# Performance work log

Measured on AMD Instinct MI355X. Metric: run time of the kernel, lower is better.

The kernel has to match this reference:

```python
import jax, jax.numpy as jnp
import numpy as np

B, T, D = 2, 2048, 1024
H, HD = 16, 64  # num_heads, key_size

def setup_inputs() -> dict:
    key = jax.random.key(0)
    ks = jax.random.split(key, 5)
    s = 1.0 / np.sqrt(D)  # VarianceScaling(1.0, fan_in) approx
    return {
        "query": jax.random.normal(ks[0], (B, T, D), dtype=jnp.float32),
        "wq": jax.random.normal(ks[1], (D, H * HD), dtype=jnp.float32) * s,
        "bq": jnp.zeros((H * HD,), dtype=jnp.float32),
        "wk": jax.random.normal(ks[2], (D, H * HD), dtype=jnp.float32) * s,
        "bk": jnp.zeros((H * HD,), dtype=jnp.float32),
        "wv": jax.random.normal(ks[3], (D, H * HD), dtype=jnp.float32) * s,
        "bv": jnp.zeros((H * HD,), dtype=jnp.float32),
        "wo": jax.random.normal(ks[4], (H * HD, D), dtype=jnp.float32) * (1.0 / np.sqrt(H * HD)),
        "bo": jnp.zeros((D,), dtype=jnp.float32),
    }

def reference(query, wq, bq, wk, bk, wv, bv, wo, bo):
    b, t, _ = query.shape
    proj = lambda w, bias: (query @ w + bias).reshape(b, t, H, HD)
    q = proj(wq, bq) / np.sqrt(HD).astype(np.float32)  # fixed scaling on queries
    k = proj(wk, bk)
    v = proj(wv, bv)
    logits = jnp.einsum('bthd,bThd->bhtT', q, k)  # [B,H,T,T]
    causal = jnp.tril(jnp.ones((t, t), dtype=logits.dtype))
    logits = logits - 1e10 * (1.0 - causal)
    weights = jax.nn.softmax(logits, axis=-1)
    attn = jnp.einsum('bhtT,bThd->bthd', weights, v)
    attn_vec = attn.reshape(b, t, H * HD)
    return attn_vec @ wo + bo
```

## Files before the change

kernel.cpp:

```cpp
#include <hip/hip_runtime.h>
#include <hip/hip_bf16.h>
#include <stdint.h>
#include <math.h>

typedef short bf16x8 __attribute__((ext_vector_type(8)));
typedef float f32x4 __attribute__((ext_vector_type(4)));
typedef __hip_bfloat16 bf16;

#define MFMA16(a, b, c) __builtin_amdgcn_mfma_f32_16x16x32_bf16((a), (b), (c), 0, 0, 0)

__device__ __forceinline__ void glds16(const void* g, void* l) {
  __builtin_amdgcn_global_load_lds((const __attribute__((address_space(1))) void*)g,
                                   (__attribute__((address_space(3))) void*)l, 16, 0, 0);
}

__device__ __forceinline__ bf16x8 ld8(const bf16* p) {
  return *reinterpret_cast<const bf16x8*>(p);
}


__global__ void k_cvt_x(const float* __restrict__ x, bf16* __restrict__ o, int n4) {
  int i = blockIdx.x * blockDim.x + threadIdx.x;
  if (i < n4) {
    float4 v = reinterpret_cast<const float4*>(x)[i];
    bf16 a0 = __float2bfloat16(v.x), a1 = __float2bfloat16(v.y);
    bf16 a2 = __float2bfloat16(v.z), a3 = __float2bfloat16(v.w);
    ushort4 r;
    r.x = reinterpret_cast<unsigned short&>(a0);
    r.y = reinterpret_cast<unsigned short&>(a1);
    r.z = reinterpret_cast<unsigned short&>(a2);
    r.w = reinterpret_cast<unsigned short&>(a3);
    reinterpret_cast<ushort4*>(o)[i] = r;
  }
}

__global__ void k_transpose_cvt(const float* __restrict__ wq, const float* __restrict__ wk,
                                const float* __restrict__ wv, const float* __restrict__ wo,
                                bf16* __restrict__ Wqkvt, bf16* __restrict__ Wot) {
  __shared__ float tile[32][33];
  const int z = blockIdx.z;
  const float* src = (z == 0) ? wq : (z == 1) ? wk : (z == 2) ? wv : wo;
  bf16* dst = (z < 3) ? (Wqkvt + (size_t)z * 1024 * 1024) : Wot;
  const int tx = threadIdx.x & 31, ty = threadIdx.x >> 5;
  const int x = blockIdx.x * 32 + tx;
  const int y0 = blockIdx.y * 32;
#pragma unroll
  for (int i = 0; i < 4; ++i) tile[ty + i * 8][tx] = src[(size_t)(y0 + ty + i * 8) * 1024 + x];
  __syncthreads();
#pragma unroll
  for (int i = 0; i < 4; ++i) {
    int c = blockIdx.x * 32 + ty + i * 8;
    dst[(size_t)c * 1024 + y0 + tx] = __float2bfloat16(tile[tx][ty + i * 8]);
  }
}


__device__ __forceinline__ void gemm_core(const bf16* __restrict__ A, const bf16* __restrict__ Bt,
                                          int K, int arow0, int bcol0,
                                          bf16* As, bf16* Bs, f32x4 acc[4][4]) {
  const int tid = threadIdx.x, lane = tid & 63, w = tid >> 6;
  const int rsub = lane >> 3, slot = lane & 7;
  const int srcslot = slot ^ rsub;
  const int wrow = (w >> 1) * 64, wcol = (w & 1) * 64;
  const int lr = lane & 15, lg = lane >> 4;
  const int nkt = K >> 6;
  for (int kt = 0; kt < nkt; ++kt) {
    const int k0 = kt * 64;
    if (kt) __syncthreads();
#pragma unroll
    for (int i = 0; i < 4; ++i) {
      const int chunk = w * 4 + i;
      glds16(A + (size_t)(arow0 + chunk * 8 + rsub) * K + k0 + srcslot * 8, As + chunk * 512);
      glds16(Bt + (size_t)(bcol0 + chunk * 8 + rsub) * K + k0 + srcslot * 8, Bs + chunk * 512);
    }
    __syncthreads();
#pragma unroll
    for (int kk = 0; kk < 2; ++kk) {
      bf16x8 af[4], bfv[4];
#pragma unroll
      for (int m = 0; m < 4; ++m) {
        const int row = wrow + m * 16 + lr;
        const int byte = (row * 128 + ((kk * 32 + lg * 8) << 1)) ^ ((row & 7) << 4);
        af[m] = *reinterpret_cast<const bf16x8*>(reinterpret_cast<const char*>(As) + byte);
      }
#pragma unroll
      for (int n = 0; n < 4; ++n) {
        const int row = wcol + n * 16 + lr;
        const int byte = (row * 128 + ((kk * 32 + lg * 8) << 1)) ^ ((row & 7) << 4);
        bfv[n] = *reinterpret_cast<const bf16x8*>(reinterpret_cast<const char*>(Bs) + byte);
      }
#pragma unroll
      for (int m = 0; m < 4; ++m)
#pragma unroll
        for (int n = 0; n < 4; ++n) acc[m][n] = MFMA16(af[m], bfv[n], acc[m][n]);
    }
  }
}


__global__ __launch_bounds__(256) void k_gemm_qkv(
    const bf16* __restrict__ X, const bf16* __restrict__ Wt,
    const float* __restrict__ bq, const float* __restrict__ bk, const float* __restrict__ bv,
    bf16* __restrict__ Qo, bf16* __restrict__ Ko, bf16* __restrict__ Vt) {
  __shared__ bf16 As[128 * 64], Bs[128 * 64];
  f32x4 acc[4][4];
#pragma unroll
  for (int i = 0; i < 4; ++i)
#pragma unroll
    for (int j = 0; j < 4; ++j) acc[i][j] = (f32x4){0.f, 0.f, 0.f, 0.f};
  const int arow0 = blockIdx.y * 128, bcol0 = blockIdx.x * 128;
  gemm_core(X, Wt, 1024, arow0, bcol0, As, Bs, acc);
  const int lane = threadIdx.x & 63, w = threadIdx.x >> 6;
  const int wrow = (w >> 1) * 64, wcol = (w & 1) * 64;
  const int lr = lane & 15, lg = lane >> 4;
  const float QSCALE = 0.125f * 1.4426950408889634f;
#pragma unroll
  for (int mi = 0; mi < 4; ++mi) {
#pragma unroll
    for (int ni = 0; ni < 4; ++ni) {
      const int r0 = arow0 + wrow + mi * 16 + lg * 4;
      const int col = bcol0 + wcol + ni * 16 + lr;
      const int which = col >> 10, cw = col & 1023, h = cw >> 6, hd = cw & 63;
      const int b = r0 >> 11, t0 = r0 & 2047;
      if (which == 2) {
        const float bias = bv[cw];
        ushort4 pk;
#pragma unroll
        for (int j = 0; j < 4; ++j) {
          bf16 hv = __float2bfloat16(acc[mi][ni][j] + bias);
          reinterpret_cast<unsigned short*>(&pk)[j] = reinterpret_cast<unsigned short&>(hv);
        }
        *reinterpret_cast<ushort4*>(Vt + ((size_t)((b * 16 + h) * 64 + hd)) * 2048 + t0) = pk;
      } else {
        const float bias = which ? bk[cw] : bq[cw];
        const float scale = which ? 1.0f : QSCALE;
        bf16* dst = which ? Ko : Qo;
#pragma unroll
        for (int j = 0; j < 4; ++j) {
          float v = (acc[mi][ni][j] + bias) * scale;
          dst[((size_t)((b * 16 + h) * 2048) + t0 + j) * 64 + hd] = __float2bfloat16(v);
        }
      }
    }
  }
}


__global__ __launch_bounds__(256) void k_attn(const bf16* __restrict__ Q, const bf16* __restrict__ Kc,
                                              const bf16* __restrict__ Vt, bf16* __restrict__ attn) {
  __shared__ bf16 Ks[2][64 * 64];
  __shared__ bf16 Vs[2][64 * 64];
  __shared__ bf16 Plds[4][16 * 64];
  const int lane = threadIdx.x & 63, w = threadIdx.x >> 6;
  const int lr = lane & 15, lg = lane >> 4;
  const int rsub = lane >> 3, slot = lane & 7;
  const int srcslot = slot ^ rsub;
  const int bh = blockIdx.x;
  const int qt = 31 - blockIdx.y;
  const int b = bh >> 4, h = bh & 15;
  const bf16* Qp = Q + (size_t)bh * 2048 * 64;
  const bf16* Kp = Kc + (size_t)bh * 2048 * 64;
  const bf16* Vp = Vt + (size_t)bh * 64 * 2048;

  const int q0 = qt * 64 + w * 16;
  const bf16x8 qa0 = ld8(Qp + (size_t)(q0 + lr) * 64 + lg * 8);
  const bf16x8 qa1 = ld8(Qp + (size_t)(q0 + lr) * 64 + 32 + lg * 8);
  f32x4 o[4];
#pragma unroll
  for (int n = 0; n < 4; ++n) o[n] = (f32x4){0.f, 0.f, 0.f, 0.f};
  float l_[4] = {0.f, 0.f, 0.f, 0.f};
  const int nkv = qt + 1;
  const float MBIAS = -8.0f * 1.4426950408889634f;
  const f32x4 minit = {MBIAS, MBIAS, MBIAS, MBIAS};

#pragma unroll
  for (int i = 0; i < 2; ++i) {
    const int ck = w * 2 + i;
    glds16(Kp + (size_t)(ck * 8 + rsub) * 64 + srcslot * 8, &Ks[0][ck * 512]);
    glds16(Vp + (size_t)(ck * 8 + rsub) * 2048 + srcslot * 8, &Vs[0][ck * 512]);
  }
  __syncthreads();
  int cur = 0;

#pragma unroll 1
  for (int it = 0; it < nkv; ++it) {
    const int kv0 = it * 64;
    if (it + 1 < nkv) {
#pragma unroll
      for (int i = 0; i < 2; ++i) {
        const int ck = w * 2 + i;
        glds16(Kp + (size_t)((it + 1) * 64 + ck * 8 + rsub) * 64 + srcslot * 8, &Ks[cur ^ 1][ck * 512]);
        glds16(Vp + (size_t)(ck * 8 + rsub) * 2048 + (it + 1) * 64 + srcslot * 8, &Vs[cur ^ 1][ck * 512]);
      }
    }
    f32x4 s[4];
    const char* Kb = reinterpret_cast<const char*>(&Ks[cur][0]);
#pragma unroll
    for (int n = 0; n < 4; ++n) {
      const int row = n * 16 + lr;
      const int rsw = (row & 7) << 4;
      bf16x8 kb0 = *reinterpret_cast<const bf16x8*>(Kb + ((row * 128 + lg * 16) ^ rsw));
      bf16x8 kb1 = *reinterpret_cast<const bf16x8*>(Kb + ((row * 128 + 64 + lg * 16) ^ rsw));
      s[n] = MFMA16(qa0, kb0, minit);
      s[n] = MFMA16(qa1, kb1, s[n]);
    }
    if (it == nkv - 1) {
#pragma unroll
      for (int n = 0; n < 4; ++n)
#pragma unroll
        for (int j = 0; j < 4; ++j)
          if (kv0 + n * 16 + lr > q0 + lg * 4 + j) s[n][j] = -1e30f;
    }
    unsigned short* Pw = reinterpret_cast<unsigned short*>(&Plds[w][0]);
#pragma unroll
    for (int n = 0; n < 4; ++n)
#pragma unroll
      for (int j = 0; j < 4; ++j) {
        float p = exp2f(s[n][j]);
        l_[j] += p;
        const int row = lg * 4 + j, col = n * 16 + lr;
        Pw[row * 64 + (col ^ ((row & 7) << 3))] = (unsigned short)(__float_as_uint(p) >> 16);
      }
    bf16x8 pa[2];
#pragma unroll
    for (int kc = 0; kc < 2; ++kc) {
      const int byte = (lr * 128 + ((kc * 32 + lg * 8) << 1)) ^ ((lr & 7) << 4);
      pa[kc] = *reinterpret_cast<const bf16x8*>(reinterpret_cast<const char*>(&Plds[w][0]) + byte);
    }
    const char* Vb = reinterpret_cast<const char*>(&Vs[cur][0]);
#pragma unroll
    for (int n2 = 0; n2 < 4; ++n2) {
#pragma unroll
      for (int kc = 0; kc < 2; ++kc) {
        const int row = n2 * 16 + lr;
        const int rsw = (row & 7) << 4;
        bf16x8 vb = *reinterpret_cast<const bf16x8*>(Vb + ((row * 128 + (kc * 32 + lg * 8) * 2) ^ rsw));
        o[n2] = MFMA16(pa[kc], vb, o[n2]);
      }
    }
    __syncthreads();
    cur ^= 1;
  }
#pragma unroll
  for (int j = 0; j < 4; ++j) {
    float v = l_[j];
#pragma unroll
    for (int off = 1; off < 16; off <<= 1) v += __shfl_xor(v, off);
    l_[j] = v;
  }
#pragma unroll
  for (int j = 0; j < 4; ++j) {
    const float inv = 1.0f / l_[j];
    const int qq = q0 + lg * 4 + j;
#pragma unroll
    for (int n2 = 0; n2 < 4; ++n2)
      attn[((size_t)(b * 2048 + qq)) * 1024 + h * 64 + n2 * 16 + lr] = __float2bfloat16(o[n2][j] * inv);
  }
}


__global__ __launch_bounds__(256) void k_gemm_out(const bf16* __restrict__ A, const bf16* __restrict__ Wot,
                                                  const float* __restrict__ bo, float* __restrict__ out) {
  __shared__ bf16 As[128 * 64], Bs[128 * 64];
  f32x4 acc[4][4];
#pragma unroll
  for (int i = 0; i < 4; ++i)
#pragma unroll
    for (int j = 0; j < 4; ++j) acc[i][j] = (f32x4){0.f, 0.f, 0.f, 0.f};
  const int arow0 = blockIdx.y * 128, bcol0 = blockIdx.x * 128;
  gemm_core(A, Wot, 1024, arow0, bcol0, As, Bs, acc);
  const int lane = threadIdx.x & 63, w = threadIdx.x >> 6;
  const int wrow = (w >> 1) * 64, wcol = (w & 1) * 64;
  const int lr = lane & 15, lg = lane >> 4;
#pragma unroll
  for (int mi = 0; mi < 4; ++mi) {
#pragma unroll
    for (int ni = 0; ni < 4; ++ni) {
      const int r0 = arow0 + wrow + mi * 16 + lg * 4;
      const int col = bcol0 + wcol + ni * 16 + lr;
      const float bias = bo[col];
#pragma unroll
      for (int j = 0; j < 4; ++j) out[(size_t)(r0 + j) * 1024 + col] = acc[mi][ni][j] + bias;
    }
  }
}


extern "C" void kernel_launch(void* const* d_in, const int* in_sizes, int n_in,
                              void* d_out, int out_size, void* d_ws, size_t ws_size,
                              hipStream_t stream) {
  const float* query = (const float*)d_in[0];
  const float* wq = (const float*)d_in[1];
  const float* bq = (const float*)d_in[2];
  const float* wk = (const float*)d_in[3];
  const float* bk = (const float*)d_in[4];
  const float* wv = (const float*)d_in[5];
  const float* bv = (const float*)d_in[6];
  const float* wo = (const float*)d_in[7];
  const float* bo = (const float*)d_in[8];
  float* out = (float*)d_out;
  char* ws = (char*)d_ws;
  const size_t MB = 1u << 20;
  bf16* X     = (bf16*)(ws + 0);
  bf16* Wqkvt = (bf16*)(ws + 8 * MB);
  bf16* Wot   = (bf16*)(ws + 14 * MB);
  bf16* Qb    = (bf16*)(ws + 16 * MB);
  bf16* Kb    = (bf16*)(ws + 24 * MB);
  bf16* Vt    = (bf16*)(ws + 32 * MB);
  bf16* attn  = (bf16*)(ws + 40 * MB);

  k_cvt_x<<<4096, 256, 0, stream>>>(query, X, 4096 * 1024 / 4);
  k_transpose_cvt<<<dim3(32, 32, 4), 256, 0, stream>>>(wq, wk, wv, wo, Wqkvt, Wot);
  k_gemm_qkv<<<dim3(24, 32), 256, 0, stream>>>(X, Wqkvt, bq, bk, bv, Qb, Kb, Vt);
  k_attn<<<dim3(32, 32), 256, 0, stream>>>(Qb, Kb, Vt, attn);
  k_gemm_out<<<dim3(8, 32), 256, 0, stream>>>(attn, Wot, bo, out);
}
```

Measured before the change: 109.4 us.

## Keep softmax P in registers via transposed QK MFMA and permlane swaps; merge prep kernels

The attention kernel swaps the operand order of the QK^T MFMA so that each lane holds scores for a single query row. The bf16 P fragments are then rearranged for the PV MFMA with v_perm and permlane32/16 swaps, replacing the round trip through the per-wave LDS P buffer. The row-sum becomes one scalar per lane, reduced across lane groups and broadcast with shuffles. Separately, the input conversion and weight transpose kernels are merged into a single launch. Together these remove LDS traffic and one kernel launch, at the cost of relying on gfx950-specific permlane instructions and a more intricate lane mapping.

```diff
diff --git a/kernel.cpp b/kernel.cpp
--- a/kernel.cpp
+++ b/kernel.cpp
@@ -5,6 +5,7 @@
 
 typedef short bf16x8 __attribute__((ext_vector_type(8)));
 typedef float f32x4 __attribute__((ext_vector_type(4)));
+typedef unsigned u32x4v __attribute__((ext_vector_type(4)));
 typedef __hip_bfloat16 bf16;
 
 #define MFMA16(a, b, c) __builtin_amdgcn_mfma_f32_16x16x32_bf16((a), (b), (c), 0, 0, 0)
@@ -18,11 +19,38 @@
   return *reinterpret_cast<const bf16x8*>(p);
 }
 
-
-__global__ void k_cvt_x(const float* __restrict__ x, bf16* __restrict__ o, int n4) {
-  int i = blockIdx.x * blockDim.x + threadIdx.x;
-  if (i < n4) {
-    float4 v = reinterpret_cast<const float4*>(x)[i];
+__device__ __forceinline__ void pl32swap(unsigned& a, unsigned& b) {
+  asm volatile("v_permlane32_swap_b32 %0, %1" : "+v"(a), "+v"(b));
+}
+__device__ __forceinline__ void pl16swap(unsigned& a, unsigned& b) {
+  asm volatile("v_permlane16_swap_b32 %0, %1" : "+v"(a), "+v"(b));
+}
+
+
+__global__ void k_prep(const float* __restrict__ query,
+                       const float* __restrict__ wq, const float* __restrict__ wk,
+                       const float* __restrict__ wv, const float* __restrict__ wo,
+                       bf16* __restrict__ X, bf16* __restrict__ Wqkvt, bf16* __restrict__ Wot) {
+  __shared__ float tile[32][33];
+  const int z = blockIdx.z;
+  if (z < 4) {
+    const float* src = (z == 0) ? wq : (z == 1) ? wk : (z == 2) ? wv : wo;
+    bf16* dst = (z < 3) ? (Wqkvt + (size_t)z * 1024 * 1024) : Wot;
+    const int tx = threadIdx.x & 31, ty = threadIdx.x >> 5;
+    const int x = blockIdx.x * 32 + tx;
+    const int y0 = blockIdx.y * 32;
+#pragma unroll
+    for (int i = 0; i < 4; ++i) tile[ty + i * 8][tx] = src[(size_t)(y0 + ty + i * 8) * 1024 + x];
+    __syncthreads();
+#pragma unroll
+    for (int i = 0; i < 4; ++i) {
+      int c = blockIdx.x * 32 + ty + i * 8;
+      dst[(size_t)c * 1024 + y0 + tx] = __float2bfloat16(tile[tx][ty + i * 8]);
+    }
+  } else {
+    const int vb = (z - 4) * 1024 + blockIdx.y * 32 + blockIdx.x;
+    const int i = vb * 256 + threadIdx.x;
+    float4 v = reinterpret_cast<const float4*>(query)[i];
     bf16 a0 = __float2bfloat16(v.x), a1 = __float2bfloat16(v.y);
     bf16 a2 = __float2bfloat16(v.z), a3 = __float2bfloat16(v.w);
     ushort4 r;
@@ -30,27 +58,7 @@
     r.y = reinterpret_cast<unsigned short&>(a1);
     r.z = reinterpret_cast<unsigned short&>(a2);
     r.w = reinterpret_cast<unsigned short&>(a3);
-    reinterpret_cast<ushort4*>(o)[i] = r;
-  }
-}
-
-__global__ void k_transpose_cvt(const float* __restrict__ wq, const float* __restrict__ wk,
-                                const float* __restrict__ wv, const float* __restrict__ wo,
-                                bf16* __restrict__ Wqkvt, bf16* __restrict__ Wot) {
-  __shared__ float tile[32][33];
-  const int z = blockIdx.z;
-  const float* src = (z == 0) ? wq : (z == 1) ? wk : (z == 2) ? wv : wo;
-  bf16* dst = (z < 3) ? (Wqkvt + (size_t)z * 1024 * 1024) : Wot;
-  const int tx = threadIdx.x & 31, ty = threadIdx.x >> 5;
-  const int x = blockIdx.x * 32 + tx;
-  const int y0 = blockIdx.y * 32;
-#pragma unroll
-  for (int i = 0; i < 4; ++i) tile[ty + i * 8][tx] = src[(size_t)(y0 + ty + i * 8) * 1024 + x];
-  __syncthreads();
-#pragma unroll
-  for (int i = 0; i < 4; ++i) {
-    int c = blockIdx.x * 32 + ty + i * 8;
-    dst[(size_t)c * 1024 + y0 + tx] = __float2bfloat16(tile[tx][ty + i * 8]);
+    reinterpret_cast<ushort4*>(X)[i] = r;
   }
 }
 
@@ -150,7 +158,6 @@
                                               const bf16* __restrict__ Vt, bf16* __restrict__ attn) {
   __shared__ bf16 Ks[2][64 * 64];
   __shared__ bf16 Vs[2][64 * 64];
-  __shared__ bf16 Plds[4][16 * 64];
   const int lane = threadIdx.x & 63, w = threadIdx.x >> 6;
   const int lr = lane & 15, lg = lane >> 4;
   const int rsub = lane >> 3, slot = lane & 7;
@@ -168,7 +175,7 @@
   f32x4 o[4];
 #pragma unroll
   for (int n = 0; n < 4; ++n) o[n] = (f32x4){0.f, 0.f, 0.f, 0.f};
-  float l_[4] = {0.f, 0.f, 0.f, 0.f};
+  float l_ = 0.f;
   const int nkv = qt + 1;
   const float MBIAS = -8.0f * 1.4426950408889634f;
   const f32x4 minit = {MBIAS, MBIAS, MBIAS, MBIAS};
@@ -201,31 +208,43 @@
       const int rsw = (row & 7) << 4;
       bf16x8 kb0 = *reinterpret_cast<const bf16x8*>(Kb + ((row * 128 + lg * 16) ^ rsw));
       bf16x8 kb1 = *reinterpret_cast<const bf16x8*>(Kb + ((row * 128 + 64 + lg * 16) ^ rsw));
-      s[n] = MFMA16(qa0, kb0, minit);
-      s[n] = MFMA16(qa1, kb1, s[n]);
+      s[n] = MFMA16(kb0, qa0, minit);
+      s[n] = MFMA16(kb1, qa1, s[n]);
     }
     if (it == nkv - 1) {
+      const int qme = q0 + lr - kv0 - lg * 4;
 #pragma unroll
       for (int n = 0; n < 4; ++n)
 #pragma unroll
         for (int j = 0; j < 4; ++j)
-          if (kv0 + n * 16 + lr > q0 + lg * 4 + j) s[n][j] = -1e30f;
-    }
-    unsigned short* Pw = reinterpret_cast<unsigned short*>(&Plds[w][0]);
+          if (n * 16 + j > qme) s[n][j] = -1e30f;
+    }
+    float p[4][4];
 #pragma unroll
     for (int n = 0; n < 4; ++n)
 #pragma unroll
       for (int j = 0; j < 4; ++j) {
-        float p = exp2f(s[n][j]);
-        l_[j] += p;
-        const int row = lg * 4 + j, col = n * 16 + lr;
-        Pw[row * 64 + (col ^ ((row & 7) << 3))] = (unsigned short)(__float_as_uint(p) >> 16);
+        p[n][j] = __builtin_amdgcn_exp2f(s[n][j]);
+        l_ += p[n][j];
+      }
+    unsigned pw[4][2];
+#pragma unroll
+    for (int n = 0; n < 4; ++n) {
+      pw[n][0] = __builtin_amdgcn_perm(__float_as_uint(p[n][1]), __float_as_uint(p[n][0]), 0x07060302u);
+      pw[n][1] = __builtin_amdgcn_perm(__float_as_uint(p[n][3]), __float_as_uint(p[n][2]), 0x07060302u);
+    }
+#pragma unroll
+    for (int n1 = 0; n1 < 2; ++n1)
+#pragma unroll
+      for (int hh = 0; hh < 2; ++hh) {
+        pl32swap(pw[2 * n1][hh], pw[2 * n1 + 1][hh]);
+        pl16swap(pw[2 * n1][hh], pw[2 * n1 + 1][hh]);
       }
     bf16x8 pa[2];
 #pragma unroll
-    for (int kc = 0; kc < 2; ++kc) {
-      const int byte = (lr * 128 + ((kc * 32 + lg * 8) << 1)) ^ ((lr & 7) << 4);
-      pa[kc] = *reinterpret_cast<const bf16x8*>(reinterpret_cast<const char*>(&Plds[w][0]) + byte);
+    for (int n1 = 0; n1 < 2; ++n1) {
+      u32x4v tv = (u32x4v){pw[2 * n1][0], pw[2 * n1][1], pw[2 * n1 + 1][0], pw[2 * n1 + 1][1]};
+      pa[n1] = __builtin_bit_cast(bf16x8, tv);
     }
     const char* Vb = reinterpret_cast<const char*>(&Vs[cur][0]);
 #pragma unroll
@@ -241,16 +260,11 @@
     __syncthreads();
     cur ^= 1;
   }
+  l_ += __shfl_xor(l_, 16);
+  l_ += __shfl_xor(l_, 32);
 #pragma unroll
   for (int j = 0; j < 4; ++j) {
-    float v = l_[j];
-#pragma unroll
-    for (int off = 1; off < 16; off <<= 1) v += __shfl_xor(v, off);
-    l_[j] = v;
-  }
-#pragma unroll
-  for (int j = 0; j < 4; ++j) {
-    const float inv = 1.0f / l_[j];
+    const float inv = 1.0f / __shfl(l_, lg * 4 + j);
     const int qq = q0 + lg * 4 + j;
 #pragma unroll
     for (int n2 = 0; n2 < 4; ++n2)
@@ -309,8 +323,7 @@
   bf16* Vt    = (bf16*)(ws + 32 * MB);
   bf16* attn  = (bf16*)(ws + 40 * MB);
 
-  k_cvt_x<<<4096, 256, 0, stream>>>(query, X, 4096 * 1024 / 4);
-  k_transpose_cvt<<<dim3(32, 32, 4), 256, 0, stream>>>(wq, wk, wv, wo, Wqkvt, Wot);
+  k_prep<<<dim3(32, 32, 8), 256, 0, stream>>>(query, wq, wk, wv, wo, X, Wqkvt, Wot);
   k_gemm_qkv<<<dim3(24, 32), 256, 0, stream>>>(X, Wqkvt, bq, bk, bv, Qb, Kb, Vt);
   k_attn<<<dim3(32, 32), 256, 0, stream>>>(Qb, Kb, Vt, attn);
   k_gemm_out<<<dim3(8, 32), 256, 0, stream>>>(attn, Wot, bo, out);
```

Measured after the change: 99.21 us. 9.3% less time.
